# Optimization experiments

Measured on AMD Instinct MI355X. Metric: run time of the kernel, lower is better.

The kernel has to match this reference:

```python
import jax, jax.numpy as jnp
import numpy as np

ALPHA = 1.0


def setup_inputs() -> dict:
    key = jax.random.key(0)
    k1, k2 = jax.random.split(key)
    N, K, D = 131072, 512, 512
    inputs = jax.random.normal(k1, (N, D), dtype=jnp.float32)
    # xavier-uniform style init for clusters
    limit = float(np.sqrt(6.0 / (K + D)))
    clusters = jax.random.uniform(k2, (K, D), dtype=jnp.float32, minval=-limit, maxval=limit)
    return {"inputs": inputs, "clusters": clusters}


def reference(inputs, clusters):
    # (same math as sum((x[:,None,:]-c)**2, -1), without the N x K x D intermediate)
    x2 = jnp.sum(inputs * inputs, axis=1, keepdims=True)          # [N, 1]
    c2 = jnp.sum(clusters * clusters, axis=1)[None, :]            # [1, K]
    d2 = jnp.maximum(x2 + c2 - 2.0 * (inputs @ clusters.T), 0.0)  # [N, K]
    q = 1.0 / (1.0 + d2 / ALPHA)
    q = q ** ((ALPHA + 1.0) / 2.0)
    return q / jnp.sum(q, axis=1, keepdims=True)
```

## Files before the change

kernel.cpp:

```cpp
#include <hip/hip_runtime.h>
#include <hip/hip_bf16.h>
#include <stdint.h>

#define NPTS 131072
#define DIM  512
#define KC   512
#define BM   64
#define BK   32
#define NKT  16

typedef float f32x16 __attribute__((ext_vector_type(16)));
typedef float f32x4  __attribute__((ext_vector_type(4)));
typedef short bf16x8 __attribute__((ext_vector_type(8)));

__device__ __forceinline__ float sq4(f32x4 a) {
  return a.x*a.x + a.y*a.y + a.z*a.z + a.w*a.w;
}

__device__ __forceinline__ bf16x8 pack8c(f32x4 a, f32x4 b) {
  union { __hip_bfloat162 h; short s[2]; } u0, u1, u2, u3;
  u0.h = __float22bfloat162_rn(make_float2(a.x, a.y));
  u1.h = __float22bfloat162_rn(make_float2(a.z, a.w));
  u2.h = __float22bfloat162_rn(make_float2(b.x, b.y));
  u3.h = __float22bfloat162_rn(make_float2(b.z, b.w));
  bf16x8 r;
  r[0] = u0.s[0]; r[1] = u0.s[1]; r[2] = u1.s[0]; r[3] = u1.s[1];
  r[4] = u2.s[0]; r[5] = u2.s[1]; r[6] = u3.s[0]; r[7] = u3.s[1];
  return r;
}

__device__ __forceinline__ short f2bf(float f) {
  union { float f; unsigned u; } v; v.f = f;
  unsigned r = v.u + 0x7FFFu + ((v.u >> 16) & 1u);
  return (short)(r >> 16);
}
__device__ __forceinline__ bf16x8 pack8(f32x4 a, f32x4 b) {
  bf16x8 p;
  p[0] = f2bf(a.x); p[1] = f2bf(a.y); p[2] = f2bf(a.z); p[3] = f2bf(a.w);
  p[4] = f2bf(b.x); p[5] = f2bf(b.y); p[6] = f2bf(b.z); p[7] = f2bf(b.w);
  return p;
}

__device__ __forceinline__ void gload_lds16(const void* g, void* l) {
  __builtin_amdgcn_global_load_lds(
      (const __attribute__((address_space(1))) unsigned int*)g,
      (__attribute__((address_space(3))) unsigned int*)l, 16, 0, 0);
}

__global__ void dec_pack(const float* __restrict__ C, short* __restrict__ Bp,
                         float* __restrict__ c2) {
  const int n    = blockIdx.x;
  const int lane = threadIdx.x;
  const float* src = C + (size_t)n * DIM + lane * 8;
  f32x4 v0 = *(const f32x4*)src;
  f32x4 v1 = *(const f32x4*)(src + 4);
  float s = sq4(v0) + sq4(v1);
  #pragma unroll
  for (int m = 1; m < 64; m <<= 1) s += __shfl_xor(s, m, 64);
  if (lane == 0) c2[n] = s;
  const int kt = lane >> 2;
  const int st = (lane >> 1) & 1;
  const int hh = lane & 1;
  const int wn = n >> 7, nt = (n >> 5) & 3, r = n & 31;
  const size_t slot =
      (((size_t)(kt * 2 + st) * 4 + wn) * 4 + nt) * 64 + hh * 32 + r;
  *(bf16x8*)(Bp + slot * 8) = pack8(v0, v1);
}

__global__ __launch_bounds__(256, 2)
void dec_main(const float* __restrict__ X, const short* __restrict__ Bp,
              const float* __restrict__ c2g, float* __restrict__ out) {
  __shared__ short Bh[3][8192];
  __shared__ float Ab[2][2048];

  const int tid  = threadIdx.x;
  const int lane = tid & 63;
  const int wn   = tid >> 6;
  const int l31  = lane & 31;
  const int h    = lane >> 5;
  const int row0 = blockIdx.x * BM;

  const int art = tid >> 3;
  const int act = tid & 7;
  const float* asrcL = X + (size_t)(row0 + art) * DIM +
                       ((act ^ (art & 7)) << 2);
  const float* asrcH = X + (size_t)(row0 + 32 + art) * DIM +
                       ((act ^ (art & 7)) << 2);
  const short* bsrc = Bp + tid * 8;

  const int asw = l31 & 7;

  f32x16 acc[2][4];
  #pragma unroll
  for (int mt = 0; mt < 2; ++mt)
    #pragma unroll
    for (int nt = 0; nt < 4; ++nt) acc[mt][nt] = (f32x16)0.f;
  float x2s[2] = {0.f, 0.f};

  #pragma unroll
  for (int sw = 0; sw < 4; ++sw)
    gload_lds16(bsrc + sw * 2048, &Bh[0][sw * 2048 + tid * 8]);
  gload_lds16(asrcL, &Ab[0][tid * 4]);
  gload_lds16(asrcH, &Ab[0][1024 + tid * 4]);
  __builtin_amdgcn_sched_barrier(0);
  #pragma unroll
  for (int sw = 0; sw < 4; ++sw)
    gload_lds16(bsrc + 8192 + sw * 2048, &Bh[1][sw * 2048 + tid * 8]);
  __builtin_amdgcn_sched_barrier(0);

  int rb = 0;
  for (int kt = 0; kt < NKT; ++kt) {
    const int rb1 = (rb == 2) ? 0 : rb + 1;
    const int rb2 = (rb == 0) ? 2 : rb - 1;

    asm volatile("s_waitcnt vmcnt(4)" ::: "memory");
    __builtin_amdgcn_sched_barrier(0);
    __builtin_amdgcn_s_barrier();
    __builtin_amdgcn_sched_barrier(0);
    {
      const int q  = (2 * kt + 2 < 32) ? 2 * kt + 2 : 31;
      const int ka = (kt + 1 < NKT) ? kt + 1 : NKT - 1;
      #pragma unroll
      for (int sw = 0; sw < 4; ++sw)
        gload_lds16(bsrc + (size_t)q * 8192 + sw * 2048,
                    &Bh[rb2][sw * 2048 + tid * 8]);
      gload_lds16(asrcL + ka * BK, &Ab[(kt + 1) & 1][tid * 4]);
      gload_lds16(asrcH + ka * BK, &Ab[(kt + 1) & 1][1024 + tid * 4]);
    }
    __builtin_amdgcn_sched_barrier(0);
    {
      const float* A = &Ab[kt & 1][0];
      bf16x8 af[2];
      #pragma unroll
      for (int mt = 0; mt < 2; ++mt) {
        f32x4 lo = *(const f32x4*)
            &A[mt * 1024 + l31 * 32 + (((h * 2 + 0) ^ asw) << 2)];
        f32x4 hi = *(const f32x4*)
            &A[mt * 1024 + l31 * 32 + (((h * 2 + 1) ^ asw) << 2)];
        x2s[mt] += sq4(lo) + sq4(hi);
        af[mt] = pack8c(lo, hi);
      }
      bf16x8 bfr[4];
      #pragma unroll
      for (int nt = 0; nt < 4; ++nt)
        bfr[nt] = *(const bf16x8*)&Bh[rb][(wn * 4 + nt) * 512 + lane * 8];
      #pragma unroll
      for (int mt = 0; mt < 2; ++mt)
        #pragma unroll
        for (int nt = 0; nt < 4; ++nt)
          acc[mt][nt] = __builtin_amdgcn_mfma_f32_32x32x16_bf16(
              af[mt], bfr[nt], acc[mt][nt], 0, 0, 0);
    }

    asm volatile("s_waitcnt vmcnt(6)" ::: "memory");
    __builtin_amdgcn_sched_barrier(0);
    __builtin_amdgcn_s_barrier();
    __builtin_amdgcn_sched_barrier(0);
    {
      const int q = (2 * kt + 3 < 32) ? 2 * kt + 3 : 31;
      #pragma unroll
      for (int sw = 0; sw < 4; ++sw)
        gload_lds16(bsrc + (size_t)q * 8192 + sw * 2048,
                    &Bh[rb][sw * 2048 + tid * 8]);
    }
    __builtin_amdgcn_sched_barrier(0);
    {
      const float* A = &Ab[kt & 1][0];
      bf16x8 af[2];
      #pragma unroll
      for (int mt = 0; mt < 2; ++mt) {
        f32x4 lo = *(const f32x4*)
            &A[mt * 1024 + l31 * 32 + (((4 + h * 2 + 0) ^ asw) << 2)];
        f32x4 hi = *(const f32x4*)
            &A[mt * 1024 + l31 * 32 + (((4 + h * 2 + 1) ^ asw) << 2)];
        x2s[mt] += sq4(lo) + sq4(hi);
        af[mt] = pack8c(lo, hi);
      }
      bf16x8 bfr[4];
      #pragma unroll
      for (int nt = 0; nt < 4; ++nt)
        bfr[nt] = *(const bf16x8*)&Bh[rb1][(wn * 4 + nt) * 512 + lane * 8];
      #pragma unroll
      for (int mt = 0; mt < 2; ++mt)
        #pragma unroll
        for (int nt = 0; nt < 4; ++nt)
          acc[mt][nt] = __builtin_amdgcn_mfma_f32_32x32x16_bf16(
              af[mt], bfr[nt], acc[mt][nt], 0, 0, 0);
    }

    rb = (rb + 2 >= 3) ? rb - 1 : rb + 2;
  }

  __syncthreads();

  #pragma unroll
  for (int mt = 0; mt < 2; ++mt) x2s[mt] += __shfl_xor(x2s[mt], 32, 64);

  float c2v[4];
  #pragma unroll
  for (int nt = 0; nt < 4; ++nt) c2v[nt] = c2g[wn * 128 + nt * 32 + l31];

  float srow[2][16];
  #pragma unroll
  for (int mt = 0; mt < 2; ++mt) {
    #pragma unroll
    for (int r = 0; r < 16; ++r) {
      const int mloc = (r & 3) + 8 * (r >> 2) + 4 * h;
      const float x2m = __shfl(x2s[mt], mloc, 64);
      float s = 0.f;
      #pragma unroll
      for (int nt = 0; nt < 4; ++nt) {
        float d2 = fmaxf(x2m + c2v[nt] - 2.f * acc[mt][nt][r], 0.f);
        float q = __builtin_amdgcn_rcpf(1.f + d2);
        acc[mt][nt][r] = q;
        s += q;
      }
      #pragma unroll
      for (int msk = 1; msk < 32; msk <<= 1) s += __shfl_xor(s, msk, 64);
      srow[mt][r] = s;
    }
  }

  float* part   = &Ab[0][0];
  float* rowinv = &Ab[0][4 * BM];

  if (l31 == 0) {
    #pragma unroll
    for (int mt = 0; mt < 2; ++mt)
      #pragma unroll
      for (int r = 0; r < 16; ++r)
        part[wn * BM + mt * 32 + (r & 3) + 8 * (r >> 2) + 4 * h] = srow[mt][r];
  }
  __syncthreads();
  if (tid < BM)
    rowinv[tid] = __builtin_amdgcn_rcpf(part[tid] + part[BM + tid] +
                                        part[2 * BM + tid] + part[3 * BM + tid]);
  __syncthreads();

  #pragma unroll
  for (int mt = 0; mt < 2; ++mt) {
    #pragma unroll
    for (int r = 0; r < 16; ++r) {
      const int row = mt * 32 + (r & 3) + 8 * (r >> 2) + 4 * h;
      const float iv = rowinv[row];
      float* o = out + (size_t)(row0 + row) * KC + wn * 128 + l31;
      #pragma unroll
      for (int nt = 0; nt < 4; ++nt)
        o[nt * 32] = acc[mt][nt][r] * iv;
    }
  }
}

extern "C" void kernel_launch(void* const* d_in, const int* in_sizes, int n_in,
                              void* d_out, int out_size, void* d_ws, size_t ws_size,
                              hipStream_t stream) {
  const float* X = (const float*)d_in[0];
  const float* C = (const float*)d_in[1];
  float* out = (float*)d_out;

  short* Bp = (short*)d_ws;
  float* c2 = (float*)((char*)d_ws + (size_t)KC * DIM * 2);

  dec_pack<<<KC, 64, 0, stream>>>(C, Bp, c2);
  dec_main<<<NPTS / BM, 256, 0, stream>>>(X, Bp, c2, out);
}
```

Measured before the change: 173.6 us.

## Double row tile to 128 with 8 waves and 4-stage pipelined K loop

```diff
diff --git a/kernel.cpp b/kernel.cpp
--- a/kernel.cpp
+++ b/kernel.cpp
@@ -5,9 +5,9 @@
 #define NPTS 131072
 #define DIM  512
 #define KC   512
-#define BM   64
-#define BK   32
-#define NKT  16
+#define BM   128
+#define BK   16
+#define NKT  32
 
 typedef float f32x16 __attribute__((ext_vector_type(16)));
 typedef float f32x4  __attribute__((ext_vector_type(4)));
@@ -67,28 +67,30 @@
   *(bf16x8*)(Bp + slot * 8) = pack8(v0, v1);
 }
 
-__global__ __launch_bounds__(256, 2)
+__global__ __launch_bounds__(512, 2)
 void dec_main(const float* __restrict__ X, const short* __restrict__ Bp,
               const float* __restrict__ c2g, float* __restrict__ out) {
-  __shared__ short Bh[3][8192];
-  __shared__ float Ab[2][2048];
+  __shared__ short Bh[4][8192];
+  __shared__ float Ah[4][2048];
+  __shared__ float part[4][BM];
+  __shared__ float rowinv[BM];
 
   const int tid  = threadIdx.x;
   const int lane = tid & 63;
-  const int wn   = tid >> 6;
+  const int wave = tid >> 6;
+  const int wm   = wave >> 2;
+  const int wn   = wave & 3;
   const int l31  = lane & 31;
   const int h    = lane >> 5;
   const int row0 = blockIdx.x * BM;
 
-  const int art = tid >> 3;
-  const int act = tid & 7;
-  const float* asrcL = X + (size_t)(row0 + art) * DIM +
-                       ((act ^ (art & 7)) << 2);
-  const float* asrcH = X + (size_t)(row0 + 32 + art) * DIM +
-                       ((act ^ (art & 7)) << 2);
+  const int art = tid >> 2;
+  const int act = tid & 3;
+  const float* asrc = X + (size_t)(row0 + art) * DIM +
+                      ((act ^ (art & 3)) << 2);
   const short* bsrc = Bp + tid * 8;
 
-  const int asw = l31 & 7;
+  const int asw = l31 & 3;
 
   f32x16 acc[2][4];
   #pragma unroll
@@ -98,52 +100,44 @@
   float x2s[2] = {0.f, 0.f};
 
   #pragma unroll
-  for (int sw = 0; sw < 4; ++sw)
-    gload_lds16(bsrc + sw * 2048, &Bh[0][sw * 2048 + tid * 8]);
-  gload_lds16(asrcL, &Ab[0][tid * 4]);
-  gload_lds16(asrcH, &Ab[0][1024 + tid * 4]);
-  __builtin_amdgcn_sched_barrier(0);
-  #pragma unroll
-  for (int sw = 0; sw < 4; ++sw)
-    gload_lds16(bsrc + 8192 + sw * 2048, &Bh[1][sw * 2048 + tid * 8]);
-  __builtin_amdgcn_sched_barrier(0);
-
-  int rb = 0;
+  for (int k0 = 0; k0 < 3; ++k0) {
+    gload_lds16(bsrc + (size_t)k0 * 8192, &Bh[k0][tid * 8]);
+    gload_lds16(bsrc + (size_t)k0 * 8192 + 4096, &Bh[k0][4096 + tid * 8]);
+    gload_lds16(asrc + k0 * BK, &Ah[k0][tid * 4]);
+    __builtin_amdgcn_sched_barrier(0);
+  }
+
   for (int kt = 0; kt < NKT; ++kt) {
-    const int rb1 = (rb == 2) ? 0 : rb + 1;
-    const int rb2 = (rb == 0) ? 2 : rb - 1;
-
-    asm volatile("s_waitcnt vmcnt(4)" ::: "memory");
+    const int sl = kt & 3;
+    const int st = (kt + 3) & 3;
+
+    asm volatile("s_waitcnt vmcnt(6)" ::: "memory");
     __builtin_amdgcn_sched_barrier(0);
     __builtin_amdgcn_s_barrier();
     __builtin_amdgcn_sched_barrier(0);
     {
-      const int q  = (2 * kt + 2 < 32) ? 2 * kt + 2 : 31;
-      const int ka = (kt + 1 < NKT) ? kt + 1 : NKT - 1;
-      #pragma unroll
-      for (int sw = 0; sw < 4; ++sw)
-        gload_lds16(bsrc + (size_t)q * 8192 + sw * 2048,
-                    &Bh[rb2][sw * 2048 + tid * 8]);
-      gload_lds16(asrcL + ka * BK, &Ab[(kt + 1) & 1][tid * 4]);
-      gload_lds16(asrcH + ka * BK, &Ab[(kt + 1) & 1][1024 + tid * 4]);
+      const int qs = (kt + 3 < NKT) ? kt + 3 : NKT - 1;
+      gload_lds16(bsrc + (size_t)qs * 8192, &Bh[st][tid * 8]);
+      gload_lds16(bsrc + (size_t)qs * 8192 + 4096, &Bh[st][4096 + tid * 8]);
+      gload_lds16(asrc + qs * BK, &Ah[st][tid * 4]);
     }
     __builtin_amdgcn_sched_barrier(0);
     {
-      const float* A = &Ab[kt & 1][0];
+      const float* A  = &Ah[sl][0];
+      const short* Bt = &Bh[sl][0];
       bf16x8 af[2];
       #pragma unroll
       for (int mt = 0; mt < 2; ++mt) {
-        f32x4 lo = *(const f32x4*)
-            &A[mt * 1024 + l31 * 32 + (((h * 2 + 0) ^ asw) << 2)];
-        f32x4 hi = *(const f32x4*)
-            &A[mt * 1024 + l31 * 32 + (((h * 2 + 1) ^ asw) << 2)];
+        const int rrb = (wm * 64 + mt * 32 + l31) * 16;
+        f32x4 lo = *(const f32x4*)&A[rrb + (((2 * h + 0) ^ asw) << 2)];
+        f32x4 hi = *(const f32x4*)&A[rrb + (((2 * h + 1) ^ asw) << 2)];
         x2s[mt] += sq4(lo) + sq4(hi);
         af[mt] = pack8c(lo, hi);
       }
       bf16x8 bfr[4];
       #pragma unroll
       for (int nt = 0; nt < 4; ++nt)
-        bfr[nt] = *(const bf16x8*)&Bh[rb][(wn * 4 + nt) * 512 + lane * 8];
+        bfr[nt] = *(const bf16x8*)&Bt[(wn * 4 + nt) * 512 + lane * 8];
       #pragma unroll
       for (int mt = 0; mt < 2; ++mt)
         #pragma unroll
@@ -151,47 +145,7 @@
           acc[mt][nt] = __builtin_amdgcn_mfma_f32_32x32x16_bf16(
               af[mt], bfr[nt], acc[mt][nt], 0, 0, 0);
     }
-
-    asm volatile("s_waitcnt vmcnt(6)" ::: "memory");
-    __builtin_amdgcn_sched_barrier(0);
-    __builtin_amdgcn_s_barrier();
-    __builtin_amdgcn_sched_barrier(0);
-    {
-      const int q = (2 * kt + 3 < 32) ? 2 * kt + 3 : 31;
-      #pragma unroll
-      for (int sw = 0; sw < 4; ++sw)
-        gload_lds16(bsrc + (size_t)q * 8192 + sw * 2048,
-                    &Bh[rb][sw * 2048 + tid * 8]);
-    }
-    __builtin_amdgcn_sched_barrier(0);
-    {
-      const float* A = &Ab[kt & 1][0];
-      bf16x8 af[2];
-      #pragma unroll
-      for (int mt = 0; mt < 2; ++mt) {
-        f32x4 lo = *(const f32x4*)
-            &A[mt * 1024 + l31 * 32 + (((4 + h * 2 + 0) ^ asw) << 2)];
-        f32x4 hi = *(const f32x4*)
-            &A[mt * 1024 + l31 * 32 + (((4 + h * 2 + 1) ^ asw) << 2)];
-        x2s[mt] += sq4(lo) + sq4(hi);
-        af[mt] = pack8c(lo, hi);
-      }
-      bf16x8 bfr[4];
-      #pragma unroll
-      for (int nt = 0; nt < 4; ++nt)
-        bfr[nt] = *(const bf16x8*)&Bh[rb1][(wn * 4 + nt) * 512 + lane * 8];
-      #pragma unroll
-      for (int mt = 0; mt < 2; ++mt)
-        #pragma unroll
-        for (int nt = 0; nt < 4; ++nt)
-          acc[mt][nt] = __builtin_amdgcn_mfma_f32_32x32x16_bf16(
-              af[mt], bfr[nt], acc[mt][nt], 0, 0, 0);
-    }
-
-    rb = (rb + 2 >= 3) ? rb - 1 : rb + 2;
-  }
-
-  __syncthreads();
+  }
 
   #pragma unroll
   for (int mt = 0; mt < 2; ++mt) x2s[mt] += __shfl_xor(x2s[mt], 32, 64);
@@ -221,27 +175,25 @@
     }
   }
 
-  float* part   = &Ab[0][0];
-  float* rowinv = &Ab[0][4 * BM];
-
   if (l31 == 0) {
     #pragma unroll
     for (int mt = 0; mt < 2; ++mt)
       #pragma unroll
       for (int r = 0; r < 16; ++r)
-        part[wn * BM + mt * 32 + (r & 3) + 8 * (r >> 2) + 4 * h] = srow[mt][r];
+        part[wn][wm * 64 + mt * 32 + (r & 3) + 8 * (r >> 2) + 4 * h] =
+            srow[mt][r];
   }
   __syncthreads();
   if (tid < BM)
-    rowinv[tid] = __builtin_amdgcn_rcpf(part[tid] + part[BM + tid] +
-                                        part[2 * BM + tid] + part[3 * BM + tid]);
+    rowinv[tid] = __builtin_amdgcn_rcpf(part[0][tid] + part[1][tid] +
+                                        part[2][tid] + part[3][tid]);
   __syncthreads();
 
   #pragma unroll
   for (int mt = 0; mt < 2; ++mt) {
     #pragma unroll
     for (int r = 0; r < 16; ++r) {
-      const int row = mt * 32 + (r & 3) + 8 * (r >> 2) + 4 * h;
+      const int row = wm * 64 + mt * 32 + (r & 3) + 8 * (r >> 2) + 4 * h;
       const float iv = rowinv[row];
       float* o = out + (size_t)(row0 + row) * KC + wn * 128 + l31;
       #pragma unroll
@@ -262,5 +214,5 @@
   float* c2 = (float*)((char*)d_ws + (size_t)KC * DIM * 2);
 
   dec_pack<<<KC, 64, 0, stream>>>(C, Bp, c2);
-  dec_main<<<NPTS / BM, 256, 0, stream>>>(X, Bp, c2, out);
-}
+  dec_main<<<NPTS / BM, 512, 0, stream>>>(X, Bp, c2, out);
+}
```

New measurement: 210.3 us. 21.2% more time.
